# Optimization experiments

Measured on AMD Instinct MI355X. Metric: run time of the kernel, lower is better.

Reference implementation:

```python
import jax, jax.numpy as jnp
import numpy as np

B, S, E = 4, 2048, 1024
H, D = 16, 64  # n_heads, head_dim; scale hardcoded as 1/sqrt(64) in source


def setup_inputs() -> dict:
    key = jax.random.key(0)
    ks = jax.random.split(key, 6)
    mk = lambda k, shp, scale=1.0: (jax.random.normal(k, shp, dtype=jnp.float32) * scale)
    return {
        "queries": mk(ks[0], (B, S, E)),
        "keys": mk(ks[1], (B, S, E)),
        "values": mk(ks[2], (B, S, E)),
        "Wq": mk(ks[3], (E, H * D), E ** -0.5),
        "Wk": mk(ks[4], (E, H * D), E ** -0.5),
        "Wv": mk(ks[5], (E, H * D), E ** -0.5),
    }


def reference(queries, keys, values, Wq, Wk, Wv):
    # linear projections
    q = jnp.einsum("bse,ef->bsf", queries, Wq).reshape(B, S, H, D)
    k = jnp.einsum("bse,ef->bsf", keys, Wk).reshape(B, S, H, D)
    v = jnp.einsum("bse,ef->bsf", values, Wv).reshape(B, S, H, D)
    # scaled dot-product attention per head (scale hardcoded to 1/sqrt(64) in source)
    scores = jnp.einsum("bqhd,bkhd->bhqk", q, k) * (1.0 / np.sqrt(64.0)).astype(np.float32)
    weights = jax.nn.softmax(scores, axis=-1)
    ctx = jnp.einsum("bhqk,bkhd->bqhd", weights, v)
    # merge heads back: [B, S, H*D]
    return ctx.reshape(B, S, H * D)
```

## Files before the change

### kernel.cpp

```cpp
#include <hip/hip_runtime.h>
#include <math.h>

#define SEQ 2048
#define EMB 1024
#define NH 16
#define HD 64
#define BH 64
#define L2E 1.44269504088896340736f

typedef __attribute__((ext_vector_type(8))) short bf16x8;
typedef __attribute__((ext_vector_type(4))) float f32x4;
typedef __attribute__((ext_vector_type(16))) float f32x16;
typedef __attribute__((ext_vector_type(4))) unsigned short u16x4;

__device__ __forceinline__ unsigned short f2bf(float f) {
  union { float fv; unsigned u; } v; v.fv = f;
  return (unsigned short)((v.u + 0x7FFFu + ((v.u >> 16) & 1u)) >> 16);
}

__device__ __forceinline__ unsigned cvt_pk_bf16(float lo, float hi) {
  unsigned r;
  asm("v_cvt_pk_bf16_f32 %0, %1, %2" : "=v"(r) : "v"(lo), "v"(hi));
  return r;
}

__device__ __forceinline__ void gl_lds16(const void* g, void* l) {
  __builtin_amdgcn_global_load_lds(
      (const __attribute__((address_space(1))) unsigned*)g,
      (__attribute__((address_space(3))) unsigned*)l, 16, 0, 0);
}

__global__ __launch_bounds__(256) void k_wt3(const float* __restrict__ Wq,
                                             const float* __restrict__ Wk,
                                             const float* __restrict__ Wv,
                                             unsigned short* __restrict__ tq,
                                             unsigned short* __restrict__ tk,
                                             unsigned short* __restrict__ tv) {
  int z = blockIdx.z;
  const float* W = (z == 0) ? Wq : (z == 1) ? Wk : Wv;
  unsigned short* Wt = (z == 0) ? tq : (z == 1) ? tk : tv;
  const float scale = (z == 0) ? 0.125f * L2E : 1.0f;

  __shared__ float tile[32][33];
  int j0 = blockIdx.x * 32, i0 = blockIdx.y * 32;
  int tx = threadIdx.x & 31, ty = threadIdx.x >> 5;
#pragma unroll
  for (int r = 0; r < 32; r += 8)
    tile[ty + r][tx] = W[(i0 + ty + r) * EMB + j0 + tx];
  __syncthreads();
#pragma unroll
  for (int r = 0; r < 32; r += 8)
    Wt[(j0 + ty + r) * EMB + i0 + tx] = f2bf(tile[tx][ty + r] * scale);
}

__global__ __launch_bounds__(256) void k_proj(
    const float* __restrict__ xq, const float* __restrict__ xk,
    const float* __restrict__ xv,
    const unsigned short* __restrict__ w0, const unsigned short* __restrict__ w1,
    const unsigned short* __restrict__ w2,
    unsigned short* __restrict__ o0, unsigned short* __restrict__ o1,
    unsigned short* __restrict__ o2) {
  int z = blockIdx.z;
  const float* X = (z == 0) ? xq : (z == 1) ? xk : xv;
  const unsigned short* Wt = (z == 0) ? w0 : (z == 1) ? w1 : w2;
  unsigned short* O = (z == 0) ? o0 : (z == 1) ? o1 : o2;

  __shared__ __align__(16) unsigned short As[2][128 * 64];
  __shared__ __align__(16) unsigned short Bs[3 * 128 * 64];

  int tid = threadIdx.x;
  int lane = tid & 63, w = tid >> 6;
  int ln15 = lane & 15, lg = lane >> 4;
  int wr = w >> 1, wc = w & 1;
  int row0 = blockIdx.x * 128, col0 = blockIdx.y * 128;

  const char* Xb = (const char*)X;
  const char* Wb = (const char*)Wt;

  f32x4 acc[4][4];
#pragma unroll
  for (int i = 0; i < 4; ++i)
#pragma unroll
    for (int j = 0; j < 4; ++j) acc[i][j] = (f32x4){0.f, 0.f, 0.f, 0.f};

  int oc[4], dswz[4];
  size_t srcA[4];
#pragma unroll
  for (int c = 0; c < 4; ++c) {
    oc[c] = w * 4096 + c * 1024 + lane * 16;
    dswz[c] = oc[c] ^ (((oc[c] >> 7) & 7) << 4);
    srcA[c] = (size_t)(row0 + (oc[c] >> 7)) * (EMB * 4) + (size_t)(oc[c] & 127) * 2;
  }
  int soB[4];
#pragma unroll
  for (int c = 0; c < 4; ++c) soB[c] = oc[c] ^ (((oc[c] >> 7) & 7) << 4);

  f32x4 arA[4][2], arB[4][2];
  auto ldA_A = [&](int kt) {
#pragma unroll
    for (int c = 0; c < 4; ++c) {
      const char* p = Xb + srcA[c] + kt * 256;
      arA[c][0] = *(const f32x4*)p;
      arA[c][1] = *(const f32x4*)(p + 16);
    }
  };
  auto ldA_B = [&](int kt) {
#pragma unroll
    for (int c = 0; c < 4; ++c) {
      const char* p = Xb + srcA[c] + kt * 256;
      arB[c][0] = *(const f32x4*)p;
      arB[c][1] = *(const f32x4*)(p + 16);
    }
  };
  auto wrA_A = [&](int buf) {
#pragma unroll
    for (int c = 0; c < 4; ++c) {
      union { unsigned u[4]; bf16x8 v; } pk;
      pk.u[0] = cvt_pk_bf16(arA[c][0][0], arA[c][0][1]);
      pk.u[1] = cvt_pk_bf16(arA[c][0][2], arA[c][0][3]);
      pk.u[2] = cvt_pk_bf16(arA[c][1][0], arA[c][1][1]);
      pk.u[3] = cvt_pk_bf16(arA[c][1][2], arA[c][1][3]);
      *(bf16x8*)((char*)As[buf] + dswz[c]) = pk.v;
    }
  };
  auto wrA_B = [&](int buf) {
#pragma unroll
    for (int c = 0; c < 4; ++c) {
      union { unsigned u[4]; bf16x8 v; } pk;
      pk.u[0] = cvt_pk_bf16(arB[c][0][0], arB[c][0][1]);
      pk.u[1] = cvt_pk_bf16(arB[c][0][2], arB[c][0][3]);
      pk.u[2] = cvt_pk_bf16(arB[c][1][0], arB[c][1][1]);
      pk.u[3] = cvt_pk_bf16(arB[c][1][2], arB[c][1][3]);
      *(bf16x8*)((char*)As[buf] + dswz[c]) = pk.v;
    }
  };
  auto stageB = [&](int slot, int kt) {
#pragma unroll
    for (int c = 0; c < 4; ++c)
      gl_lds16(Wb + (size_t)(col0 + (soB[c] >> 7)) * (EMB * 2) + kt * 128 + (soB[c] & 127),
               (char*)Bs + slot * 16384 + w * 4096 + c * 1024);
  };

  auto mfmaStep = [&](int cur, int bslot) {
    const char* bbase = (const char*)Bs + bslot * 16384;
#pragma unroll
    for (int ks = 0; ks < 2; ++ks) {
      bf16x8 a[4], bb[4];
#pragma unroll
      for (int i = 0; i < 4; ++i) {
        int row = wr * 64 + i * 16 + ln15;
        int ba = (row * 128 + ks * 64 + lg * 16) ^ ((row & 7) << 4);
        a[i] = *(const bf16x8*)((const char*)As[cur] + ba);
      }
#pragma unroll
      for (int j = 0; j < 4; ++j) {
        int row = wc * 64 + j * 16 + ln15;
        int ba = (row * 128 + ks * 64 + lg * 16) ^ ((row & 7) << 4);
        bb[j] = *(const bf16x8*)(bbase + ba);
      }
      __builtin_amdgcn_s_setprio(1);
#pragma unroll
      for (int i = 0; i < 4; ++i)
#pragma unroll
        for (int j = 0; j < 4; ++j)
          acc[i][j] = __builtin_amdgcn_mfma_f32_16x16x32_bf16(a[i], bb[j], acc[i][j], 0, 0, 0);
      __builtin_amdgcn_s_setprio(0);
    }
  };

  auto vbar = [&]() {
    asm volatile("s_waitcnt vmcnt(12) lgkmcnt(0)" ::: "memory");
    __builtin_amdgcn_s_barrier();
    __builtin_amdgcn_sched_barrier(0);
  };

  ldA_A(0);
  stageB(0, 0);
  stageB(1, 1);
  wrA_A(0);
  ldA_B(1);
  vbar();

#pragma unroll
  for (int kp = 0; kp < 8; ++kp) {
    const int kte = 2 * kp;
    if (kte + 2 <= 15) stageB((kte + 2) % 3, kte + 2);
    if (kte < 14) ldA_A(kte + 2);
    mfmaStep(0, kte % 3);
    wrA_B(1);
    vbar();

    const int kto = 2 * kp + 1;
    if (kto + 2 <= 15) stageB((kto + 2) % 3, kto + 2);
    if (kto < 14) ldA_B(kto + 2);
    mfmaStep(1, kto % 3);
    if (kto < 15) wrA_A(0);
    vbar();
  }

  if (z == 2) {
#pragma unroll
    for (int i = 0; i < 4; ++i) {
#pragma unroll
      for (int j = 0; j < 4; ++j) {
        int col = col0 + wc * 64 + j * 16 + ln15;
        int h = col >> 6, d = col & 63;
        int rowb = row0 + wr * 64 + i * 16 + lg * 4;
        int b = rowb >> 11, s = rowb & (SEQ - 1);
        u16x4 hv;
#pragma unroll
        for (int r = 0; r < 4; ++r) hv[r] = f2bf(acc[i][j][r]);
        *(u16x4*)&O[(((size_t)(b * NH + h) * HD) + d) * SEQ + s] = hv;
      }
    }
  } else {
#pragma unroll
    for (int i = 0; i < 4; ++i) {
#pragma unroll
      for (int j = 0; j < 4; ++j) {
#pragma unroll
        for (int r = 0; r < 4; ++r) {
          int row = row0 + wr * 64 + i * 16 + lg * 4 + r;
          int col = col0 + wc * 64 + j * 16 + ln15;
          int b = row >> 11, s = row & (SEQ - 1);
          int h = col >> 6, d = col & 63;
          O[(((size_t)(b * NH + h) * SEQ) + s) * HD + d] = f2bf(acc[i][j][r]);
        }
      }
    }
  }
}

__global__ __launch_bounds__(512) void k_attn(const unsigned short* __restrict__ Q,
                                              const unsigned short* __restrict__ K,
                                              const unsigned short* __restrict__ Vt,
                                              float* __restrict__ out) {
  __shared__ __align__(16) unsigned short Klds[2 * 32 * 64];
  __shared__ __align__(16) unsigned short Vlds[2 * 64 * 64];

  const int id = blockIdx.x;
  const int swz = (id & 7) * 64 + (id >> 3);
  const int bh = swz >> 3, qb = swz & 7;
  const int b = bh >> 4, h = bh & 15;

  const int tid = threadIdx.x;
  const int w = tid >> 6, lane = tid & 63;
  const int q31 = lane & 31;
  const int hi = lane >> 5;
  const int q0 = qb * 256 + w * 32;

  const unsigned short* Qb = Q + (size_t)bh * SEQ * HD;
  const char* Kb = (const char*)(K + (size_t)bh * SEQ * HD);
  const char* Vb = (const char*)(Vt + (size_t)bh * HD * SEQ);

  bf16x8 qf[4];
#pragma unroll
  for (int kk = 0; kk < 4; ++kk)
    qf[kk] = *(const bf16x8*)&Qb[(q0 + q31) * HD + kk * 16 + hi * 8];

  f32x16 ctx[2];
#pragma unroll
  for (int db = 0; db < 2; ++db)
#pragma unroll
    for (int r = 0; r < 16; ++r) ctx[db][r] = 0.f;

  f32x16 zero16;
#pragma unroll
  for (int r = 0; r < 16; ++r) zero16[r] = 0.f;
  union { unsigned u[4]; bf16x8 v; } onesf;
#pragma unroll
  for (int r = 0; r < 4; ++r) onesf.u[r] = 0x3F803F80u;
  f32x16 lsum = zero16;

  const int sw = (q31 & 7) << 4;
  int kaddr[4];
#pragma unroll
  for (int kk = 0; kk < 4; ++kk)
    kaddr[kk] = q31 * 128 + (((kk * 32) | (hi * 16)) ^ sw);
  int vaddr[2][2];
#pragma unroll
  for (int pi = 0; pi < 2; ++pi)
#pragma unroll
    for (int j = 0; j < 2; ++j)
      vaddr[pi][j] = q31 * 128 + (((pi * 64) | (j * 32) | (hi * 16)) ^ sw);

  const int o0 = w * 1024 + lane * 16;
  const int os0 = o0 ^ (((o0 >> 7) & 7) << 4);

  auto stageK = [&](int slot, int kt) {
    if (w < 4)
      gl_lds16(Kb + (size_t)kt * 4096 + os0, (char*)Klds + slot * 4096 + w * 1024);
  };
  auto stageV = [&](int slot, int vt) {
    gl_lds16(Vb + (size_t)(os0 >> 7) * (SEQ * 2) + vt * 128 + (os0 & 127),
             (char*)Vlds + slot * 8192 + w * 1024);
  };

  auto barrierC = [&]() {
    if (w < 4) asm volatile("s_waitcnt vmcnt(1)" ::: "memory");
    __builtin_amdgcn_s_barrier();
    __builtin_amdgcn_sched_barrier(0);
  };

  auto qk = [&](f32x16& sx, const char* kbase) {
    __builtin_amdgcn_s_setprio(1);
    bf16x8 kf0 = *(const bf16x8*)(kbase + kaddr[0]);
    sx = __builtin_amdgcn_mfma_f32_32x32x16_bf16(kf0, qf[0], zero16, 0, 0, 0);
#pragma unroll
    for (int kk = 1; kk < 4; ++kk) {
      bf16x8 kf = *(const bf16x8*)(kbase + kaddr[kk]);
      sx = __builtin_amdgcn_mfma_f32_32x32x16_bf16(kf, qf[kk], sx, 0, 0, 0);
    }
    __builtin_amdgcn_s_setprio(0);
  };

  auto smpv = [&](f32x16& sx, int pinIdx, int vb) {
#pragma unroll
    for (int r = 0; r < 16; ++r) sx[r] = __builtin_amdgcn_exp2f(sx[r]);

    unsigned a0 = cvt_pk_bf16(sx[0], sx[1]);
    unsigned a1 = cvt_pk_bf16(sx[2], sx[3]);
    unsigned a2 = cvt_pk_bf16(sx[4], sx[5]);
    unsigned a3 = cvt_pk_bf16(sx[6], sx[7]);
    unsigned a4 = cvt_pk_bf16(sx[8], sx[9]);
    unsigned a5 = cvt_pk_bf16(sx[10], sx[11]);
    unsigned a6 = cvt_pk_bf16(sx[12], sx[13]);
    unsigned a7 = cvt_pk_bf16(sx[14], sx[15]);
    asm volatile("v_permlane32_swap_b32 %0, %1" : "+v"(a0), "+v"(a2));
    asm volatile("v_permlane32_swap_b32 %0, %1" : "+v"(a1), "+v"(a3));
    asm volatile("v_permlane32_swap_b32 %0, %1" : "+v"(a4), "+v"(a6));
    asm volatile("v_permlane32_swap_b32 %0, %1" : "+v"(a5), "+v"(a7));
    union { unsigned u[4]; bf16x8 v; } pa_lo, pa_hi;
    pa_lo.u[0] = a0; pa_lo.u[1] = a1; pa_lo.u[2] = a2; pa_lo.u[3] = a3;
    pa_hi.u[0] = a4; pa_hi.u[1] = a5; pa_hi.u[2] = a6; pa_hi.u[3] = a7;

    const char* vbp = (const char*)Vlds + vb;
    __builtin_amdgcn_s_setprio(1);
    lsum = __builtin_amdgcn_mfma_f32_32x32x16_bf16(pa_lo.v, onesf.v, lsum, 0, 0, 0);
    lsum = __builtin_amdgcn_mfma_f32_32x32x16_bf16(pa_hi.v, onesf.v, lsum, 0, 0, 0);
#pragma unroll
    for (int db = 0; db < 2; ++db) {
      bf16x8 v0 = *(const bf16x8*)(vbp + db * 4096 + vaddr[pinIdx][0]);
      bf16x8 v1 = *(const bf16x8*)(vbp + db * 4096 + vaddr[pinIdx][1]);
      ctx[db] = __builtin_amdgcn_mfma_f32_32x32x16_bf16(pa_lo.v, v0, ctx[db], 0, 0, 0);
      ctx[db] = __builtin_amdgcn_mfma_f32_32x32x16_bf16(pa_hi.v, v1, ctx[db], 0, 0, 0);
    }
    __builtin_amdgcn_s_setprio(0);
  };

  const char* K0 = (const char*)Klds;
  const char* K1 = (const char*)Klds + 4096;
  f32x16 sA, sB;

  stageK(0, 0);
  stageV(0, 0);
  barrierC();
  qk(sA, K0);
  stageK(1, 1);
  __syncthreads();

  for (int tp = 0; tp < 31; ++tp) {
    const int vb = (tp & 1) << 13;
    qk(sB, K1);
    stageK(0, 2 * tp + 2);
    stageV((tp + 1) & 1, tp + 1);
    smpv(sA, 0, vb);
    barrierC();
    qk(sA, K0);
    stageK(1, 2 * tp + 3);
    smpv(sB, 1, vb);
    __syncthreads();
  }
  qk(sB, K1);
  smpv(sA, 0, 8192);
  smpv(sB, 1, 8192);

#pragma unroll
  for (int db = 0; db < 2; ++db) {
#pragma unroll
    for (int r = 0; r < 16; ++r) {
      int q = q0 + (r & 3) + 8 * (r >> 2) + 4 * hi;
      out[((size_t)b * SEQ + q) * (NH * HD) + h * HD + db * 32 + q31] =
          ctx[db][r] / lsum[r];
    }
  }
}

extern "C" void kernel_launch(void* const* d_in, const int* in_sizes, int n_in,
                              void* d_out, int out_size, void* d_ws, size_t ws_size,
                              hipStream_t stream) {
  (void)in_sizes; (void)n_in; (void)out_size; (void)ws_size;
  const float* queries = (const float*)d_in[0];
  const float* keys    = (const float*)d_in[1];
  const float* values  = (const float*)d_in[2];
  const float* Wq = (const float*)d_in[3];
  const float* Wk = (const float*)d_in[4];
  const float* Wv = (const float*)d_in[5];
  float* out = (float*)d_out;

  char* ws = (char*)d_ws;
  const size_t MB = 1024 * 1024;
  unsigned short* q_ws = (unsigned short*)(ws);
  unsigned short* k_ws = (unsigned short*)(ws + 16 * MB);
  unsigned short* v_ws = (unsigned short*)(ws + 32 * MB);
  unsigned short* wtq  = (unsigned short*)(ws + 48 * MB);
  unsigned short* wtk  = (unsigned short*)(ws + 50 * MB);
  unsigned short* wtv  = (unsigned short*)(ws + 52 * MB);

  k_wt3<<<dim3(32, 32, 3), 256, 0, stream>>>(Wq, Wk, Wv, wtq, wtk, wtv);
  k_proj<<<dim3(64, 8, 3), 256, 0, stream>>>(queries, keys, values,
                                             wtq, wtk, wtv, q_ws, k_ws, v_ws);
  k_attn<<<dim3(512), 512, 0, stream>>>(q_ws, k_ws, v_ws, out);
}
```

Measured before the change: 159.5 us.

## Restructure attention K/V pipeline to stage two K tiles per barrier

Doubles the K LDS buffer to four slots so all eight waves stage K, each half loading a different tile, and each barrier phase now covers two K tiles and one V tile. This halves the number of barriers per iteration and removes the partial vmcnt wait, which is meant to cut synchronisation overhead and idle waves during staging. The cost is more LDS per block and a loop that is no longer unrolled. The final loads may also be exposed with less overlap against compute.

```diff
diff --git a/kernel.cpp b/kernel.cpp
--- a/kernel.cpp
+++ b/kernel.cpp
@@ -235,7 +235,7 @@
                                               const unsigned short* __restrict__ K,
                                               const unsigned short* __restrict__ Vt,
                                               float* __restrict__ out) {
-  __shared__ __align__(16) unsigned short Klds[2 * 32 * 64];
+  __shared__ __align__(16) unsigned short Klds[4 * 32 * 64];
   __shared__ __align__(16) unsigned short Vlds[2 * 64 * 64];
 
   const int id = blockIdx.x;
@@ -245,6 +245,7 @@
 
   const int tid = threadIdx.x;
   const int w = tid >> 6, lane = tid & 63;
+  const int wk = w & 3;
   const int q31 = lane & 31;
   const int hi = lane >> 5;
   const int q0 = qb * 256 + w * 32;
@@ -284,22 +285,19 @@
     for (int j = 0; j < 2; ++j)
       vaddr[pi][j] = q31 * 128 + (((pi * 64) | (j * 32) | (hi * 16)) ^ sw);
 
-  const int o0 = w * 1024 + lane * 16;
-  const int os0 = o0 ^ (((o0 >> 7) & 7) << 4);
-
-  auto stageK = [&](int slot, int kt) {
-    if (w < 4)
-      gl_lds16(Kb + (size_t)kt * 4096 + os0, (char*)Klds + slot * 4096 + w * 1024);
+  const int ok = wk * 1024 + lane * 16;
+  const int osk = ok ^ (((ok >> 7) & 7) << 4);
+  const int ov = w * 1024 + lane * 16;
+  const int osv = ov ^ (((ov >> 7) & 7) << 4);
+
+  auto stageK2 = [&](int slotE, int ktE, int slotO, int ktO) {
+    const int slot = (w < 4) ? slotE : slotO;
+    const int kt = (w < 4) ? ktE : ktO;
+    gl_lds16(Kb + (size_t)kt * 4096 + osk, (char*)Klds + slot * 4096 + wk * 1024);
   };
   auto stageV = [&](int slot, int vt) {
-    gl_lds16(Vb + (size_t)(os0 >> 7) * (SEQ * 2) + vt * 128 + (os0 & 127),
+    gl_lds16(Vb + (size_t)(osv >> 7) * (SEQ * 2) + vt * 128 + (osv & 127),
              (char*)Vlds + slot * 8192 + w * 1024);
-  };
-
-  auto barrierC = [&]() {
-    if (w < 4) asm volatile("s_waitcnt vmcnt(1)" ::: "memory");
-    __builtin_amdgcn_s_barrier();
-    __builtin_amdgcn_sched_barrier(0);
   };
 
   auto qk = [&](f32x16& sx, const char* kbase) {
@@ -348,32 +346,36 @@
     __builtin_amdgcn_s_setprio(0);
   };
 
-  const char* K0 = (const char*)Klds;
-  const char* K1 = (const char*)Klds + 4096;
+  const char* KS0 = (const char*)Klds;
+  const char* KS1 = (const char*)Klds + 4096;
+  const char* KS2 = (const char*)Klds + 8192;
+  const char* KS3 = (const char*)Klds + 12288;
   f32x16 sA, sB;
 
-  stageK(0, 0);
+  stageK2(0, 0, 1, 1);
   stageV(0, 0);
-  barrierC();
-  qk(sA, K0);
-  stageK(1, 1);
   __syncthreads();
 
-  for (int tp = 0; tp < 31; ++tp) {
-    const int vb = (tp & 1) << 13;
-    qk(sB, K1);
-    stageK(0, 2 * tp + 2);
-    stageV((tp + 1) & 1, tp + 1);
-    smpv(sA, 0, vb);
-    barrierC();
-    qk(sA, K0);
-    stageK(1, 2 * tp + 3);
-    smpv(sB, 1, vb);
+#pragma unroll 1
+  for (int tpp = 0; tpp < 16; ++tpp) {
+    const int t0 = 4 * tpp;
+    qk(sA, KS0);
+    stageK2(2, t0 + 2, 3, t0 + 3);
+    stageV(1, 2 * tpp + 1);
+    smpv(sA, 0, 0);
+    qk(sB, KS1);
+    smpv(sB, 1, 0);
+    __syncthreads();
+    qk(sA, KS2);
+    if (tpp < 15) {
+      stageK2(0, t0 + 4, 1, t0 + 5);
+      stageV(0, 2 * tpp + 2);
+    }
+    smpv(sA, 0, 8192);
+    qk(sB, KS3);
+    smpv(sB, 1, 8192);
     __syncthreads();
   }
-  qk(sB, K1);
-  smpv(sA, 0, 8192);
-  smpv(sB, 1, 8192);
 
 #pragma unroll
   for (int db = 0; db < 2; ++db) {
```

Result: no change. 160.6 us (+0.7%).

## Split attention KV range across two blocks and combine partial results

Applied to the files above, without the earlier changes.

The attention kernel now splits each query block's key/value sequence into two halves, launching twice as many blocks, and each writes unnormalized partial context and row sums to workspace. A new combine kernel adds the two partials and divides by the summed normalizer. The aim is better occupancy of the 256 CUs, since 512 blocks of 512 threads left parallelism thin. The cost is an extra launch plus roughly 64MB of fp32 partial writes and reads. This only works without max-rescaling because the softmax appears to use no running max, so the partials combine directly.

```diff
diff --git a/kernel.cpp b/kernel.cpp
--- a/kernel.cpp
+++ b/kernel.cpp
@@ -234,14 +234,18 @@
 __global__ __launch_bounds__(512) void k_attn(const unsigned short* __restrict__ Q,
                                               const unsigned short* __restrict__ K,
                                               const unsigned short* __restrict__ Vt,
-                                              float* __restrict__ out) {
+                                              float* __restrict__ pctx,
+                                              float* __restrict__ pl) {
   __shared__ __align__(16) unsigned short Klds[2 * 32 * 64];
   __shared__ __align__(16) unsigned short Vlds[2 * 64 * 64];
 
   const int id = blockIdx.x;
-  const int swz = (id & 7) * 64 + (id >> 3);
-  const int bh = swz >> 3, qb = swz & 7;
-  const int b = bh >> 4, h = bh & 15;
+  const int swz = (id & 7) * 128 + (id >> 3);
+  const int bh = swz >> 4;
+  const int qb = (swz >> 1) & 7;
+  const int half = swz & 1;
+  const int kt0 = half * 32;
+  const int vt0 = half * 16;
 
   const int tid = threadIdx.x;
   const int w = tid >> 6, lane = tid & 63;
@@ -352,22 +356,22 @@
   const char* K1 = (const char*)Klds + 4096;
   f32x16 sA, sB;
 
-  stageK(0, 0);
-  stageV(0, 0);
+  stageK(0, kt0);
+  stageV(0, vt0);
   barrierC();
   qk(sA, K0);
-  stageK(1, 1);
+  stageK(1, kt0 + 1);
   __syncthreads();
 
-  for (int tp = 0; tp < 31; ++tp) {
+  for (int tp = 0; tp < 15; ++tp) {
     const int vb = (tp & 1) << 13;
     qk(sB, K1);
-    stageK(0, 2 * tp + 2);
-    stageV((tp + 1) & 1, tp + 1);
+    stageK(0, kt0 + 2 * tp + 2);
+    stageV((tp + 1) & 1, vt0 + tp + 1);
     smpv(sA, 0, vb);
     barrierC();
     qk(sA, K0);
-    stageK(1, 2 * tp + 3);
+    stageK(1, kt0 + 2 * tp + 3);
     smpv(sB, 1, vb);
     __syncthreads();
   }
@@ -375,15 +379,42 @@
   smpv(sA, 0, 8192);
   smpv(sB, 1, 8192);
 
+  float* pc = pctx + ((size_t)(half * BH + bh) * SEQ) * HD;
 #pragma unroll
   for (int db = 0; db < 2; ++db) {
 #pragma unroll
     for (int r = 0; r < 16; ++r) {
       int q = q0 + (r & 3) + 8 * (r >> 2) + 4 * hi;
-      out[((size_t)b * SEQ + q) * (NH * HD) + h * HD + db * 32 + q31] =
-          ctx[db][r] / lsum[r];
-    }
-  }
+      pc[(size_t)q * HD + db * 32 + q31] = ctx[db][r];
+    }
+  }
+  if (q31 == 0) {
+    float* plb = pl + (size_t)(half * BH + bh) * SEQ;
+#pragma unroll
+    for (int r = 0; r < 16; ++r) {
+      int q = q0 + (r & 3) + 8 * (r >> 2) + 4 * hi;
+      plb[q] = lsum[r];
+    }
+  }
+}
+
+__global__ __launch_bounds__(256) void k_comb(const float* __restrict__ pctx,
+                                              const float* __restrict__ pl,
+                                              float* __restrict__ out) {
+  const size_t HALF = (size_t)BH * SEQ * HD;
+  int idx = blockIdx.x * 256 + threadIdx.x;
+  int bh = idx >> 15;
+  int q = (idx >> 4) & (SEQ - 1);
+  int dc = idx & 15;
+  size_t o = ((size_t)bh * SEQ + q) * HD + dc * 4;
+  f32x4 c0 = *(const f32x4*)(pctx + o);
+  f32x4 c1 = *(const f32x4*)(pctx + HALF + o);
+  float li = 1.0f / (pl[(size_t)bh * SEQ + q] + pl[(size_t)(BH + bh) * SEQ + q]);
+  int b = bh >> 4, h = bh & 15;
+  f32x4 rv;
+#pragma unroll
+  for (int j = 0; j < 4; ++j) rv[j] = (c0[j] + c1[j]) * li;
+  *(f32x4*)(out + ((size_t)(b * SEQ + q)) * (NH * HD) + h * HD + dc * 4) = rv;
 }
 
 extern "C" void kernel_launch(void* const* d_in, const int* in_sizes, int n_in,
@@ -406,9 +437,12 @@
   unsigned short* wtq  = (unsigned short*)(ws + 48 * MB);
   unsigned short* wtk  = (unsigned short*)(ws + 50 * MB);
   unsigned short* wtv  = (unsigned short*)(ws + 52 * MB);
+  float* pctx = (float*)(ws + 56 * MB);
+  float* pl   = (float*)(ws + 120 * MB);
 
   k_wt3<<<dim3(32, 32, 3), 256, 0, stream>>>(Wq, Wk, Wv, wtq, wtk, wtv);
   k_proj<<<dim3(64, 8, 3), 256, 0, stream>>>(queries, keys, values,
                                              wtq, wtk, wtv, q_ws, k_ws, v_ws);
-  k_attn<<<dim3(512), 512, 0, stream>>>(q_ws, k_ws, v_ws, out);
-}
+  k_attn<<<dim3(1024), 512, 0, stream>>>(q_ws, k_ws, v_ws, pctx, pl);
+  k_comb<<<dim3(8192), 256, 0, stream>>>(pctx, pl, out);
+}
```

New measurement: 185.2 us. 16.1% more time.
